# Performance work log

Measured on AMD Instinct MI355X. Metric: run time of the kernel, lower is better.

Reference implementation:

```python
import jax, jax.numpy as jnp
import numpy as np

N = 100000
E = 1600000
IN_C, HID_C, OUT_C = 128, 64, 32


def _add_self_loops(edge_index, n):
    loops = jnp.arange(n, dtype=edge_index.dtype)
    src = jnp.concatenate([edge_index[0], loops])
    dst = jnp.concatenate([edge_index[1], loops])
    return src, dst


def _gcn_norm(src, dst, n):
    # symmetric normalization on A + I with unit edge weights
    deg = jax.ops.segment_sum(jnp.ones_like(dst, dtype=jnp.float32), dst, num_segments=n)
    dinv = jnp.where(deg > 0, jax.lax.rsqrt(deg), 0.0)
    return dinv[src] * dinv[dst]  # [E+N]


def _gcn_conv(x, src, dst, norm, W, b, n):
    h = x @ W                              # [N, out]
    msg = h[src] * norm[:, None]           # [E+N, out]  (dominant gather)
    out = jax.ops.segment_sum(msg, dst, num_segments=n)
    return out + b


def setup_inputs() -> dict:
    key = jax.random.key(0)
    k = jax.random.split(key, 6)
    x = jax.random.normal(k[0], (N, IN_C), dtype=jnp.float32)
    edge_index = jax.random.randint(k[1], (2, E), 0, N, dtype=jnp.int32)
    # Glorot-style init for GCN weights
    W1 = jax.random.normal(k[2], (IN_C, HID_C), dtype=jnp.float32) / np.sqrt(IN_C)
    b1 = jnp.zeros((HID_C,), dtype=jnp.float32)
    W2 = jax.random.normal(k[3], (HID_C, OUT_C), dtype=jnp.float32) / np.sqrt(HID_C)
    b2 = jnp.zeros((OUT_C,), dtype=jnp.float32)
    return {"x": x, "edge_index": edge_index, "W1": W1, "b1": b1, "W2": W2, "b2": b2}


def reference(x, edge_index, W1, b1, W2, b2):
    src, dst = _add_self_loops(edge_index, N)
    norm = _gcn_norm(src, dst, N)
    h = _gcn_conv(x, src, dst, norm, W1, b1, N)
    h = jax.nn.relu(h)
    # dropout p=0.2 is identity in eval mode
    out = _gcn_conv(h, src, dst, norm, W2, b2, N)
    return out
```

## Files before the change

kernel.cpp:

```cpp
#include <hip/hip_runtime.h>
#include <hip/hip_fp16.h>

#define N_NODES 100000
#define E_EDGES 1600000
#define IN_C 128
#define HID_C 64
#define OUT_C 32
#define BNODES 64
#define NBUCK ((N_NODES + BNODES - 1) / BNODES)
#define MAXB 2048
#define NCHUNK 256
#define CHUNK_E (E_EDGES / NCHUNK)

__device__ __forceinline__ int chunk_of_block(int b) { return (b & 7) * (NCHUNK / 8) + (b >> 3); }

__global__ void zero_gcur_kernel(int* __restrict__ gcur) {
    int i = blockIdx.x * 256 + threadIdx.x;
    if (i < NBUCK) gcur[i] = 0;
}

__global__ __launch_bounds__(1024) void bucket_scatter_kernel(const int* __restrict__ src,
                                                              const int* __restrict__ dst,
                                                              int* __restrict__ gcur,
                                                              unsigned* __restrict__ pairs) {
    __shared__ int h[NBUCK];
    for (int i = threadIdx.x; i < NBUCK; i += 1024) h[i] = 0;
    __syncthreads();
    const int chunk = chunk_of_block(blockIdx.x);
    const int base = chunk * CHUNK_E;
    int dc[7];
    int nj = 0;
    for (int j = threadIdx.x; j < CHUNK_E; j += 1024) {
        int d = dst[base + j];
        dc[nj++] = d;
        atomicAdd(&h[d >> 6], 1);
    }
    __syncthreads();
    for (int i = threadIdx.x; i < NBUCK; i += 1024) {
        int c = h[i];
        if (c > 0) h[i] = atomicAdd(&gcur[i], c);
    }
    __syncthreads();
    nj = 0;
    for (int j = threadIdx.x; j < CHUNK_E; j += 1024) {
        int d = dc[nj++];
        int pos = atomicAdd(&h[d >> 6], 1);
        pairs[(unsigned)(d >> 6) * MAXB + (unsigned)pos] =
            ((unsigned)src[base + j] << 6) | (unsigned)(d & 63);
    }
}

__global__ __launch_bounds__(256) void bucket_sort_kernel(const int* __restrict__ gcur,
                                                          unsigned* __restrict__ pairs,
                                                          int* __restrict__ row_beg,
                                                          int* __restrict__ row_end,
                                                          float* __restrict__ dinv) {
    __shared__ unsigned sp[MAXB];
    __shared__ int hcnt[BNODES], scn[BNODES], cur[BNODES];
    const int b = blockIdx.x;
    const int beg = b * MAXB;
    int cnt = gcur[b];
    if (cnt > MAXB) cnt = MAXB;
    if (threadIdx.x < BNODES) hcnt[threadIdx.x] = 0;
    __syncthreads();
    for (int j = threadIdx.x; j < cnt; j += 256) {
        unsigned p = pairs[beg + j];
        sp[j] = p;
        atomicAdd(&hcnt[p & 63], 1);
    }
    __syncthreads();
    if (threadIdx.x < BNODES) scn[threadIdx.x] = hcnt[threadIdx.x];
    __syncthreads();
    for (int off = 1; off < BNODES; off <<= 1) {
        int t = 0;
        if (threadIdx.x < BNODES && threadIdx.x >= off) t = scn[threadIdx.x - off];
        __syncthreads();
        if (threadIdx.x < BNODES) scn[threadIdx.x] += t;
        __syncthreads();
    }
    if (threadIdx.x < BNODES) {
        int ex = scn[threadIdx.x] - hcnt[threadIdx.x];
        cur[threadIdx.x] = ex;
        int node = b * BNODES + threadIdx.x;
        if (node < N_NODES) {
            row_beg[node] = beg + ex;
            row_end[node] = beg + ex + hcnt[threadIdx.x];
            dinv[node] = rsqrtf((float)hcnt[threadIdx.x] + 1.0f);
        }
    }
    __syncthreads();
    for (int j = threadIdx.x; j < cnt; j += 256) {
        unsigned p = sp[j];
        int pos = atomicAdd(&cur[p & 63], 1);
        pairs[beg + pos] = p >> 6;
    }
}

__global__ __launch_bounds__(256) void gemm1_kernel(const float* __restrict__ x,
                                                    const float* __restrict__ W1,
                                                    const float* __restrict__ dinv,
                                                    __half* __restrict__ hs) {
    __shared__ float sW[IN_C * HID_C];
    for (int i = threadIdx.x; i < IN_C * HID_C; i += 256) sW[i] = W1[i];
    __syncthreads();
    const int cg = (threadIdx.x & 7) * 8;
    const int row0 = blockIdx.x * 128 + (threadIdx.x >> 3) * 4;
    float acc[4][8];
#pragma unroll
    for (int r = 0; r < 4; ++r)
#pragma unroll
        for (int c = 0; c < 8; ++c) acc[r][c] = 0.f;

    int rr[4];
#pragma unroll
    for (int r = 0; r < 4; ++r) rr[r] = min(row0 + r, N_NODES - 1);

    const float4* x4 = (const float4*)x;
#pragma unroll 2
    for (int k4 = 0; k4 < IN_C / 4; ++k4) {
        float4 xv[4];
#pragma unroll
        for (int r = 0; r < 4; ++r) xv[r] = x4[(size_t)rr[r] * (IN_C / 4) + k4];
        float xs[4][4];
#pragma unroll
        for (int r = 0; r < 4; ++r) {
            xs[r][0] = xv[r].x; xs[r][1] = xv[r].y; xs[r][2] = xv[r].z; xs[r][3] = xv[r].w;
        }
#pragma unroll
        for (int kk = 0; kk < 4; ++kk) {
            const float4* wp = (const float4*)(sW + (k4 * 4 + kk) * HID_C + cg);
            float4 w0 = wp[0], w1 = wp[1];
            float wv[8] = {w0.x, w0.y, w0.z, w0.w, w1.x, w1.y, w1.z, w1.w};
#pragma unroll
            for (int r = 0; r < 4; ++r)
#pragma unroll
                for (int c = 0; c < 8; ++c)
                    acc[r][c] = fmaf(xs[r][kk], wv[c], acc[r][c]);
        }
    }
#pragma unroll
    for (int r = 0; r < 4; ++r) {
        int row = row0 + r;
        if (row < N_NODES) {
            float dv = dinv[row];
            union { float4 f; __half2 h[4]; } u;
#pragma unroll
            for (int q = 0; q < 4; ++q)
                u.h[q] = __floats2half2_rn(acc[r][2 * q] * dv, acc[r][2 * q + 1] * dv);
            *(float4*)(hs + (size_t)row * HID_C + cg) = u.f;
        }
    }
}

__global__ void agg1_kernel(const int* __restrict__ row_beg, const int* __restrict__ row_end,
                            const int* __restrict__ col,
                            const __half2* __restrict__ hs2, const float* __restrict__ dinv,
                            const float* __restrict__ b1, __half2* __restrict__ h2h) {
    const int node = blockIdx.x * 8 + (threadIdx.x >> 5);
    const int c2 = threadIdx.x & 31;
    if (node >= N_NODES) return;
    const int beg = row_beg[node], end = row_end[node];
    float2 f = __half22float2(hs2[node * 32 + c2]);
    float ax = f.x, ay = f.y;
    int j = beg;
    for (; j + 7 < end; j += 8) {
        int s0 = col[j],     s1 = col[j + 1], s2 = col[j + 2], s3 = col[j + 3];
        int s4 = col[j + 4], s5 = col[j + 5], s6 = col[j + 6], s7 = col[j + 7];
        float2 v0 = __half22float2(hs2[s0 * 32 + c2]);
        float2 v1 = __half22float2(hs2[s1 * 32 + c2]);
        float2 v2 = __half22float2(hs2[s2 * 32 + c2]);
        float2 v3 = __half22float2(hs2[s3 * 32 + c2]);
        float2 v4 = __half22float2(hs2[s4 * 32 + c2]);
        float2 v5 = __half22float2(hs2[s5 * 32 + c2]);
        float2 v6 = __half22float2(hs2[s6 * 32 + c2]);
        float2 v7 = __half22float2(hs2[s7 * 32 + c2]);
        ax += ((v0.x + v1.x) + (v2.x + v3.x)) + ((v4.x + v5.x) + (v6.x + v7.x));
        ay += ((v0.y + v1.y) + (v2.y + v3.y)) + ((v4.y + v5.y) + (v6.y + v7.y));
    }
    for (; j + 1 < end; j += 2) {
        int s0 = col[j], s1 = col[j + 1];
        float2 v0 = __half22float2(hs2[s0 * 32 + c2]);
        float2 v1 = __half22float2(hs2[s1 * 32 + c2]);
        ax += v0.x + v1.x; ay += v0.y + v1.y;
    }
    if (j < end) {
        float2 v = __half22float2(hs2[col[j] * 32 + c2]);
        ax += v.x; ay += v.y;
    }
    float dv = dinv[node];
    float2 bb = ((const float2*)b1)[c2];
    h2h[node * 32 + c2] = __floats2half2_rn(fmaxf(dv * ax + bb.x, 0.f),
                                            fmaxf(dv * ay + bb.y, 0.f));
}

__global__ __launch_bounds__(256) void gemm2_kernel(const __half* __restrict__ h2h,
                                                    const float* __restrict__ W2,
                                                    const float* __restrict__ dinv,
                                                    __half* __restrict__ gs) {
    __shared__ float sW[HID_C * OUT_C];
    for (int i = threadIdx.x; i < HID_C * OUT_C; i += 256) sW[i] = W2[i];
    __syncthreads();
    const int cg = (threadIdx.x & 3) * 8;
    const int row0 = blockIdx.x * 128 + (threadIdx.x >> 2) * 2;
    float acc[2][8];
#pragma unroll
    for (int r = 0; r < 2; ++r)
#pragma unroll
        for (int c = 0; c < 8; ++c) acc[r][c] = 0.f;

    int rr[2];
#pragma unroll
    for (int r = 0; r < 2; ++r) rr[r] = min(row0 + r, N_NODES - 1);

    const float4* h4 = (const float4*)h2h;
    for (int k8 = 0; k8 < HID_C / 8; ++k8) {
        float xs[2][8];
#pragma unroll
        for (int r = 0; r < 2; ++r) {
            union { float4 f; __half2 h[4]; } u;
            u.f = h4[(size_t)rr[r] * (HID_C / 8) + k8];
#pragma unroll
            for (int q = 0; q < 4; ++q) {
                float2 v = __half22float2(u.h[q]);
                xs[r][2 * q] = v.x; xs[r][2 * q + 1] = v.y;
            }
        }
#pragma unroll
        for (int kk = 0; kk < 8; ++kk) {
            const float4* wp = (const float4*)(sW + (k8 * 8 + kk) * OUT_C + cg);
            float4 w0 = wp[0], w1 = wp[1];
            float wv[8] = {w0.x, w0.y, w0.z, w0.w, w1.x, w1.y, w1.z, w1.w};
#pragma unroll
            for (int r = 0; r < 2; ++r)
#pragma unroll
                for (int c = 0; c < 8; ++c)
                    acc[r][c] = fmaf(xs[r][kk], wv[c], acc[r][c]);
        }
    }
#pragma unroll
    for (int r = 0; r < 2; ++r) {
        int row = row0 + r;
        if (row < N_NODES) {
            float dv = dinv[row];
            union { float4 f; __half2 h[4]; } u;
#pragma unroll
            for (int q = 0; q < 4; ++q)
                u.h[q] = __floats2half2_rn(acc[r][2 * q] * dv, acc[r][2 * q + 1] * dv);
            *(float4*)(gs + (size_t)row * OUT_C + cg) = u.f;
        }
    }
}

__global__ void agg2_kernel(const int* __restrict__ row_beg, const int* __restrict__ row_end,
                            const int* __restrict__ col,
                            const __half2* __restrict__ gs2, const float* __restrict__ dinv,
                            const float* __restrict__ b2, float* __restrict__ out) {
    const int node = blockIdx.x * 16 + (threadIdx.x >> 4);
    const int c2 = threadIdx.x & 15;
    if (node >= N_NODES) return;
    const int beg = row_beg[node], end = row_end[node];
    float2 f = __half22float2(gs2[node * 16 + c2]);
    float ax = f.x, ay = f.y;
    int j = beg;
    for (; j + 7 < end; j += 8) {
        int s0 = col[j],     s1 = col[j + 1], s2 = col[j + 2], s3 = col[j + 3];
        int s4 = col[j + 4], s5 = col[j + 5], s6 = col[j + 6], s7 = col[j + 7];
        float2 v0 = __half22float2(gs2[s0 * 16 + c2]);
        float2 v1 = __half22float2(gs2[s1 * 16 + c2]);
        float2 v2 = __half22float2(gs2[s2 * 16 + c2]);
        float2 v3 = __half22float2(gs2[s3 * 16 + c2]);
        float2 v4 = __half22float2(gs2[s4 * 16 + c2]);
        float2 v5 = __half22float2(gs2[s5 * 16 + c2]);
        float2 v6 = __half22float2(gs2[s6 * 16 + c2]);
        float2 v7 = __half22float2(gs2[s7 * 16 + c2]);
        ax += ((v0.x + v1.x) + (v2.x + v3.x)) + ((v4.x + v5.x) + (v6.x + v7.x));
        ay += ((v0.y + v1.y) + (v2.y + v3.y)) + ((v4.y + v5.y) + (v6.y + v7.y));
    }
    for (; j + 1 < end; j += 2) {
        int s0 = col[j], s1 = col[j + 1];
        float2 v0 = __half22float2(gs2[s0 * 16 + c2]);
        float2 v1 = __half22float2(gs2[s1 * 16 + c2]);
        ax += v0.x + v1.x; ay += v0.y + v1.y;
    }
    if (j < end) {
        float2 v = __half22float2(gs2[col[j] * 16 + c2]);
        ax += v.x; ay += v.y;
    }
    float dv = dinv[node];
    float2 bb = ((const float2*)b2)[c2];
    float2 o;
    o.x = dv * ax + bb.x;
    o.y = dv * ay + bb.y;
    ((float2*)out)[node * 16 + c2] = o;
}

extern "C" void kernel_launch(void* const* d_in, const int* in_sizes, int n_in,
                              void* d_out, int out_size, void* d_ws, size_t ws_size,
                              hipStream_t stream) {
    const float* x  = (const float*)d_in[0];
    const int*   ei = (const int*)d_in[1];
    const float* W1 = (const float*)d_in[2];
    const float* b1 = (const float*)d_in[3];
    const float* W2 = (const float*)d_in[4];
    const float* b2 = (const float*)d_in[5];
    float* out = (float*)d_out;

    const int* srcv = ei;
    const int* dstv = ei + E_EDGES;

    float* dinv  = (float*)d_ws;
    __half* hs   = (__half*)(dinv + N_NODES);
    __half* h2h  = hs + (size_t)N_NODES * HID_C;
    int* row_beg = (int*)(h2h + (size_t)N_NODES * HID_C);
    int* row_end = row_beg + N_NODES;
    int* gcur    = row_end + N_NODES;
    unsigned* pairs = (unsigned*)(gcur + 1568);
    __half* gs = hs;
    int* col = (int*)pairs;

    zero_gcur_kernel<<<(NBUCK + 255) / 256, 256, 0, stream>>>(gcur);
    bucket_scatter_kernel<<<NCHUNK, 1024, 0, stream>>>(srcv, dstv, gcur, pairs);
    bucket_sort_kernel<<<NBUCK, 256, 0, stream>>>(gcur, pairs, row_beg, row_end, dinv);

    gemm1_kernel<<<(N_NODES + 127) / 128, 256, 0, stream>>>(x, W1, dinv, hs);
    agg1_kernel<<<(N_NODES + 7) / 8, 256, 0, stream>>>(row_beg, row_end, col,
                                                       (const __half2*)hs, dinv, b1,
                                                       (__half2*)h2h);

    gemm2_kernel<<<(N_NODES + 127) / 128, 256, 0, stream>>>(h2h, W2, dinv, gs);
    agg2_kernel<<<(N_NODES + 15) / 16, 256, 0, stream>>>(row_beg, row_end, col,
                                                         (const __half2*)gs, dinv, b2, out);
}
```

Measured before the change: 144.3 us.

## Split feature matrices into channel slices so gathers hit smaller working sets

Stores the hidden features (hs, h2h) and layer-2 features in a sliced layout: four slices of 16 or 8 channels, each contiguous over all nodes. The aggregation kernels give each block one slice, with block indices interleaved so co-resident blocks work on the same slice, and threads handle fewer channels per node. The aim is a smaller per-slice gather working set that fits in L2/MALL and gets better cache hit rates for random neighbour gathers. In exchange, each edge's column index is read four times, and each gather is a narrow 32- or 16-byte segment.

```diff
diff --git a/kernel.cpp b/kernel.cpp
--- a/kernel.cpp
+++ b/kernel.cpp
@@ -138,6 +138,8 @@
                     acc[r][c] = fmaf(xs[r][kk], wv[c], acc[r][c]);
         }
     }
+    const int sl = cg >> 4;
+    const int off = cg & 15;
 #pragma unroll
     for (int r = 0; r < 4; ++r) {
         int row = row0 + r;
@@ -147,7 +149,7 @@
 #pragma unroll
             for (int q = 0; q < 4; ++q)
                 u.h[q] = __floats2half2_rn(acc[r][2 * q] * dv, acc[r][2 * q + 1] * dv);
-            *(float4*)(hs + (size_t)row * HID_C + cg) = u.f;
+            *(float4*)(hs + ((size_t)sl * N_NODES + row) * 16 + off) = u.f;
         }
     }
 }
@@ -156,41 +158,45 @@
                             const int* __restrict__ col,
                             const __half2* __restrict__ hs2, const float* __restrict__ dinv,
                             const float* __restrict__ b1, __half2* __restrict__ h2h) {
-    const int node = blockIdx.x * 8 + (threadIdx.x >> 5);
-    const int c2 = threadIdx.x & 31;
+    const int g = blockIdx.x & 7;
+    const int slice = g >> 1;
+    const int ngi = (blockIdx.x >> 3) * 2 + (g & 1);
+    const int node = ngi * 32 + (threadIdx.x >> 3);
+    const int c2 = threadIdx.x & 7;
     if (node >= N_NODES) return;
+    const size_t sb = (size_t)slice * N_NODES;
     const int beg = row_beg[node], end = row_end[node];
-    float2 f = __half22float2(hs2[node * 32 + c2]);
+    float2 f = __half22float2(hs2[(sb + node) * 8 + c2]);
     float ax = f.x, ay = f.y;
     int j = beg;
     for (; j + 7 < end; j += 8) {
         int s0 = col[j],     s1 = col[j + 1], s2 = col[j + 2], s3 = col[j + 3];
         int s4 = col[j + 4], s5 = col[j + 5], s6 = col[j + 6], s7 = col[j + 7];
-        float2 v0 = __half22float2(hs2[s0 * 32 + c2]);
-        float2 v1 = __half22float2(hs2[s1 * 32 + c2]);
-        float2 v2 = __half22float2(hs2[s2 * 32 + c2]);
-        float2 v3 = __half22float2(hs2[s3 * 32 + c2]);
-        float2 v4 = __half22float2(hs2[s4 * 32 + c2]);
-        float2 v5 = __half22float2(hs2[s5 * 32 + c2]);
-        float2 v6 = __half22float2(hs2[s6 * 32 + c2]);
-        float2 v7 = __half22float2(hs2[s7 * 32 + c2]);
+        float2 v0 = __half22float2(hs2[(sb + s0) * 8 + c2]);
+        float2 v1 = __half22float2(hs2[(sb + s1) * 8 + c2]);
+        float2 v2 = __half22float2(hs2[(sb + s2) * 8 + c2]);
+        float2 v3 = __half22float2(hs2[(sb + s3) * 8 + c2]);
+        float2 v4 = __half22float2(hs2[(sb + s4) * 8 + c2]);
+        float2 v5 = __half22float2(hs2[(sb + s5) * 8 + c2]);
+        float2 v6 = __half22float2(hs2[(sb + s6) * 8 + c2]);
+        float2 v7 = __half22float2(hs2[(sb + s7) * 8 + c2]);
         ax += ((v0.x + v1.x) + (v2.x + v3.x)) + ((v4.x + v5.x) + (v6.x + v7.x));
         ay += ((v0.y + v1.y) + (v2.y + v3.y)) + ((v4.y + v5.y) + (v6.y + v7.y));
     }
     for (; j + 1 < end; j += 2) {
         int s0 = col[j], s1 = col[j + 1];
-        float2 v0 = __half22float2(hs2[s0 * 32 + c2]);
-        float2 v1 = __half22float2(hs2[s1 * 32 + c2]);
+        float2 v0 = __half22float2(hs2[(sb + s0) * 8 + c2]);
+        float2 v1 = __half22float2(hs2[(sb + s1) * 8 + c2]);
         ax += v0.x + v1.x; ay += v0.y + v1.y;
     }
     if (j < end) {
-        float2 v = __half22float2(hs2[col[j] * 32 + c2]);
+        float2 v = __half22float2(hs2[(sb + col[j]) * 8 + c2]);
         ax += v.x; ay += v.y;
     }
     float dv = dinv[node];
-    float2 bb = ((const float2*)b1)[c2];
-    h2h[node * 32 + c2] = __floats2half2_rn(fmaxf(dv * ax + bb.x, 0.f),
-                                            fmaxf(dv * ay + bb.y, 0.f));
+    float2 bb = ((const float2*)b1)[slice * 8 + c2];
+    h2h[(sb + node) * 8 + c2] = __floats2half2_rn(fmaxf(dv * ax + bb.x, 0.f),
+                                                  fmaxf(dv * ay + bb.y, 0.f));
 }
 
 __global__ __launch_bounds__(256) void gemm2_kernel(const __half* __restrict__ h2h,
@@ -218,7 +224,7 @@
 #pragma unroll
         for (int r = 0; r < 2; ++r) {
             union { float4 f; __half2 h[4]; } u;
-            u.f = h4[(size_t)rr[r] * (HID_C / 8) + k8];
+            u.f = h4[((size_t)(k8 >> 1) * N_NODES + rr[r]) * 2 + (k8 & 1)];
 #pragma unroll
             for (int q = 0; q < 4; ++q) {
                 float2 v = __half22float2(u.h[q]);
@@ -237,6 +243,7 @@
                     acc[r][c] = fmaf(xs[r][kk], wv[c], acc[r][c]);
         }
     }
+    const int sl = threadIdx.x & 3;
 #pragma unroll
     for (int r = 0; r < 2; ++r) {
         int row = row0 + r;
@@ -246,7 +253,7 @@
 #pragma unroll
             for (int q = 0; q < 4; ++q)
                 u.h[q] = __floats2half2_rn(acc[r][2 * q] * dv, acc[r][2 * q + 1] * dv);
-            *(float4*)(gs + (size_t)row * OUT_C + cg) = u.f;
+            *(float4*)(gs + ((size_t)sl * N_NODES + row) * 8) = u.f;
         }
     }
 }
@@ -255,43 +262,47 @@
                             const int* __restrict__ col,
                             const __half2* __restrict__ gs2, const float* __restrict__ dinv,
                             const float* __restrict__ b2, float* __restrict__ out) {
-    const int node = blockIdx.x * 16 + (threadIdx.x >> 4);
-    const int c2 = threadIdx.x & 15;
+    const int g = blockIdx.x & 7;
+    const int slice = g >> 1;
+    const int ngi = (blockIdx.x >> 3) * 2 + (g & 1);
+    const int node = ngi * 64 + (threadIdx.x >> 2);
+    const int c2 = threadIdx.x & 3;
     if (node >= N_NODES) return;
+    const size_t sb = (size_t)slice * N_NODES;
     const int beg = row_beg[node], end = row_end[node];
-    float2 f = __half22float2(gs2[node * 16 + c2]);
+    float2 f = __half22float2(gs2[(sb + node) * 4 + c2]);
     float ax = f.x, ay = f.y;
     int j = beg;
     for (; j + 7 < end; j += 8) {
         int s0 = col[j],     s1 = col[j + 1], s2 = col[j + 2], s3 = col[j + 3];
         int s4 = col[j + 4], s5 = col[j + 5], s6 = col[j + 6], s7 = col[j + 7];
-        float2 v0 = __half22float2(gs2[s0 * 16 + c2]);
-        float2 v1 = __half22float2(gs2[s1 * 16 + c2]);
-        float2 v2 = __half22float2(gs2[s2 * 16 + c2]);
-        float2 v3 = __half22float2(gs2[s3 * 16 + c2]);
-        float2 v4 = __half22float2(gs2[s4 * 16 + c2]);
-        float2 v5 = __half22float2(gs2[s5 * 16 + c2]);
-        float2 v6 = __half22float2(gs2[s6 * 16 + c2]);
-        float2 v7 = __half22float2(gs2[s7 * 16 + c2]);
+        float2 v0 = __half22float2(gs2[(sb + s0) * 4 + c2]);
+        float2 v1 = __half22float2(gs2[(sb + s1) * 4 + c2]);
+        float2 v2 = __half22float2(gs2[(sb + s2) * 4 + c2]);
+        float2 v3 = __half22float2(gs2[(sb + s3) * 4 + c2]);
+        float2 v4 = __half22float2(gs2[(sb + s4) * 4 + c2]);
+        float2 v5 = __half22float2(gs2[(sb + s5) * 4 + c2]);
+        float2 v6 = __half22float2(gs2[(sb + s6) * 4 + c2]);
+        float2 v7 = __half22float2(gs2[(sb + s7) * 4 + c2]);
         ax += ((v0.x + v1.x) + (v2.x + v3.x)) + ((v4.x + v5.x) + (v6.x + v7.x));
         ay += ((v0.y + v1.y) + (v2.y + v3.y)) + ((v4.y + v5.y) + (v6.y + v7.y));
     }
     for (; j + 1 < end; j += 2) {
         int s0 = col[j], s1 = col[j + 1];
-        float2 v0 = __half22float2(gs2[s0 * 16 + c2]);
-        float2 v1 = __half22float2(gs2[s1 * 16 + c2]);
+        float2 v0 = __half22float2(gs2[(sb + s0) * 4 + c2]);
+        float2 v1 = __half22float2(gs2[(sb + s1) * 4 + c2]);
         ax += v0.x + v1.x; ay += v0.y + v1.y;
     }
     if (j < end) {
-        float2 v = __half22float2(gs2[col[j] * 16 + c2]);
+        float2 v = __half22float2(gs2[(sb + col[j]) * 4 + c2]);
         ax += v.x; ay += v.y;
     }
     float dv = dinv[node];
-    float2 bb = ((const float2*)b2)[c2];
+    float2 bb = ((const float2*)b2)[slice * 4 + c2];
     float2 o;
     o.x = dv * ax + bb.x;
     o.y = dv * ay + bb.y;
-    ((float2*)out)[node * 16 + c2] = o;
+    ((float2*)out)[(size_t)node * 16 + slice * 4 + c2] = o;
 }
 
 extern "C" void kernel_launch(void* const* d_in, const int* in_sizes, int n_in,
@@ -323,11 +334,10 @@
     bucket_sort_kernel<<<NBUCK, 256, 0, stream>>>(gcur, pairs, row_beg, row_end, dinv);
 
     gemm1_kernel<<<(N_NODES + 127) / 128, 256, 0, stream>>>(x, W1, dinv, hs);
-    agg1_kernel<<<(N_NODES + 7) / 8, 256, 0, stream>>>(row_beg, row_end, col,
-                                                       (const __half2*)hs, dinv, b1,
-                                                       (__half2*)h2h);
+    agg1_kernel<<<1563 * 8, 256, 0, stream>>>(row_beg, row_end, col, (const __half2*)hs,
+                                              dinv, b1, (__half2*)h2h);
 
     gemm2_kernel<<<(N_NODES + 127) / 128, 256, 0, stream>>>(h2h, W2, dinv, gs);
-    agg2_kernel<<<(N_NODES + 15) / 16, 256, 0, stream>>>(row_beg, row_end, col,
-                                                         (const __half2*)gs, dinv, b2, out);
-}
+    agg2_kernel<<<782 * 8, 256, 0, stream>>>(row_beg, row_end, col, (const __half2*)gs,
+                                             dinv, b2, out);
+}
```

After: 167.5 us. 16.1% more time.
